# Optimization experiments

Hardware: AMD Instinct MI355X
Metric: run time of the kernel (lower is better)

## Reference

```python
import jax, jax.numpy as jnp
import numpy as np

B, N0, FEAT, NHID, GDIM = 32, 2048, 1036, 128, 32
DEG = 16
E = B * N0 * DEG
K1, K2, K3 = 410, 82, 17  # ceil(0.2*{2048,410,82}) per SAGPooling stage


def _segsum(v, idx, n):
    return jax.ops.segment_sum(v, idx, num_segments=n)


def sage_conv(x, src, dst, em, Wl, bl, Wr, n):
    # PyG SAGEConv: lin_l(mean_{j->i} x_j) + lin_r(x_i); lin applied before the
    # (linear) mean -> identical math, messages are NHID-dim not FEAT-dim.
    h = x @ Wl
    s = _segsum(h[src] * em[:, None], dst, n)
    cnt = _segsum(em, dst, n)
    return s / jnp.maximum(cnt, 1.0)[:, None] + bl + x @ Wr


def gcn_score(x, src, dst, em, W, b, n):
    # 1-channel GCNConv with self-loops and symmetric normalization.
    h = x @ W  # [n, 1]
    deg = 1.0 + _segsum(em, dst, n)  # +1 for self loop
    dis = jax.lax.rsqrt(deg)
    norm = dis[src] * dis[dst] * em
    agg = _segsum(h[src] * norm[:, None], dst, n) + h / deg[:, None]
    return (agg + b)[:, 0]


def sag_pool(x, src, dst, em, W, b, n_per, k):
    # Equal-size graphs -> static top-k per graph; dropped edges masked, not removed.
    nb = x.shape[0] // n_per
    score = gcn_score(x, src, dst, em, W, b, x.shape[0])
    _, idx = jax.lax.top_k(score.reshape(nb, n_per), k)
    perm = (idx + (jnp.arange(nb) * n_per)[:, None]).reshape(-1)
    xn = x[perm] * jnp.tanh(score[perm])[:, None]
    inv = jnp.full((x.shape[0],), -1, jnp.int32).at[perm].set(
        jnp.arange(nb * k, dtype=jnp.int32))
    ns, nd = inv[src], inv[dst]
    emn = em * ((ns >= 0) & (nd >= 0)).astype(em.dtype)
    return xn, jnp.maximum(ns, 0), jnp.maximum(nd, 0), emn


def readout(x, k):
    r = x.reshape(B, k, NHID)
    return jnp.concatenate([r.max(axis=1), r.mean(axis=1)], axis=1)  # [B, 2*NHID]


def graphnet(x, src, dst, W1l, b1l, W1r, Wp1, bp1, W2l, b2l, W2r, Wp2, bp2,
             W3l, b3l, W3r, Wp3, bp3, lin1_w, lin1_b, lin2_w, lin2_b, lin3_w, lin3_b):
    # NormalizeFeaturesV2: first 12 cols / column max
    mx = jnp.max(x[:, :12], axis=0)
    x = jnp.concatenate([x[:, :12] / mx, x[:, 12:]], axis=1)
    em = jnp.ones((E,), x.dtype)

    x = jax.nn.relu(sage_conv(x, src, dst, em, W1l, b1l, W1r, B * N0))
    x, s1, d1, e1 = sag_pool(x, src, dst, em, Wp1, bp1, N0, K1)
    x1 = readout(x, K1)

    x = jax.nn.relu(sage_conv(x, s1, d1, e1, W2l, b2l, W2r, B * K1))
    x, s2, d2, e2 = sag_pool(x, s1, d1, e1, Wp2, bp2, K1, K2)
    x2 = readout(x, K2)

    x = jax.nn.relu(sage_conv(x, s2, d2, e2, W3l, b3l, W3r, B * K2))
    x, s3, d3, e3 = sag_pool(x, s2, d2, e2, Wp3, bp3, K2, K3)
    x3 = readout(x, K3)

    h = x1 + x2 + x3
    h = jax.nn.relu(h @ lin1_w + lin1_b)  # dropout is identity at eval
    features = jax.nn.relu(h @ lin2_w + lin2_b)
    out = features @ lin3_w + lin3_b  # act=None
    return features, out


def setup_inputs():
    key = jax.random.key(0)
    ks = jax.random.split(key, 16)
    x = jax.random.normal(ks[0], (B * N0, FEAT), jnp.float32)
    e = jax.random.randint(ks[1], (2, B, N0 * DEG), 0, N0)
    ei = (e + (jnp.arange(B) * N0)[None, :, None]).reshape(2, -1).astype(jnp.int32)

    def lin(k, fi, fo):
        return (jax.random.normal(k, (fi, fo), jnp.float32) / np.sqrt(fi)).astype(jnp.float32)

    z = lambda *s: jnp.zeros(s, jnp.float32)
    return dict(
        x=x, src=ei[0], dst=ei[1],
        W1l=lin(ks[2], FEAT, NHID), b1l=z(NHID), W1r=lin(ks[3], FEAT, NHID),
        Wp1=lin(ks[4], NHID, 1), bp1=z(1),
        W2l=lin(ks[5], NHID, NHID), b2l=z(NHID), W2r=lin(ks[6], NHID, NHID),
        Wp2=lin(ks[7], NHID, 1), bp2=z(1),
        W3l=lin(ks[8], NHID, NHID), b3l=z(NHID), W3r=lin(ks[9], NHID, NHID),
        Wp3=lin(ks[10], NHID, 1), bp3=z(1),
        lin1_w=lin(ks[11], 2 * NHID, NHID), lin1_b=z(NHID),
        lin2_w=lin(ks[12], NHID, GDIM), lin2_b=z(GDIM),
        lin3_w=lin(ks[13], GDIM, 1), lin3_b=z(1),
    )


def reference(x, src, dst, W1l, b1l, W1r, Wp1, bp1, W2l, b2l, W2r, Wp2, bp2,
              W3l, b3l, W3r, Wp3, bp3, lin1_w, lin1_b, lin2_w, lin2_b, lin3_w, lin3_b):
    return graphnet(x, src, dst, W1l, b1l, W1r, Wp1, bp1, W2l, b2l, W2r, Wp2, bp2,
                    W3l, b3l, W3r, Wp3, bp3, lin1_w, lin1_b, lin2_w, lin2_b,
                    lin3_w, lin3_b)
```

## Files before the change

kernel.cpp:

```cpp
#include <hip/hip_runtime.h>

typedef unsigned int u32;
typedef unsigned short u16;

#define NB 32
#define N0V 2048
#define FEATV 1036
#define EDGESV (NB*N0V*16)
#define KK1 410
#define KK2 82
#define KK3 17
#define NN1 (NB*N0V)
#define NN2 (NB*KK1)
#define NN3 (NB*KK2)
#define NN4 (NB*KK3)
#define KSTEP1 33
#define KSTEP2 4
#define ESTR 32768

typedef __bf16 bf16x8 __attribute__((ext_vector_type(8)));
typedef float f32x4 __attribute__((ext_vector_type(4)));

__device__ inline u16 f2bf(float f){
  u32 u = __float_as_uint(f);
  u32 r = (u + 0x7FFFu + ((u >> 16) & 1u)) >> 16;
  return (u16)r;
}
__device__ inline float bf2f(u16 h){ return __uint_as_float(((u32)h) << 16); }
__device__ inline float dec_ord(u32 u){
  u32 bits = (u & 0x80000000u) ? (u ^ 0x80000000u) : ~u;
  return __uint_as_float(bits);
}
__device__ inline u16 bfbits(__bf16 b){ union{__bf16 f; u16 u;} c; c.f=b; return c.u; }
__device__ inline void cvt4c(float4 v, ushort4& h, ushort4& l){
  __bf16 h0=(__bf16)v.x, h1=(__bf16)v.y, h2=(__bf16)v.z, h3=(__bf16)v.w;
  float r0=v.x-(float)h0, r1=v.y-(float)h1, r2=v.z-(float)h2, r3=v.w-(float)h3;
  h.x=bfbits(h0); h.y=bfbits(h1); h.z=bfbits(h2); h.w=bfbits(h3);
  l.x=bfbits((__bf16)r0); l.y=bfbits((__bf16)r1);
  l.z=bfbits((__bf16)r2); l.w=bfbits((__bf16)r3);
}
__device__ inline void gload_lds16(const void* g, void* l){
  __builtin_amdgcn_global_load_lds(
      (const __attribute__((address_space(1))) unsigned int*)g,
      (__attribute__((address_space(3))) unsigned int*)l, 16, 0, 0);
}

__global__ void init_kernel(u32* mx){
  if (threadIdx.x < 12) mx[threadIdx.x] = 0;
}

__global__ void colmax_kernel(const float* __restrict__ x, u32* mx){
  __shared__ float sm[256];
  int t = threadIdx.x;
  int r = blockIdx.x*256 + t;
  const float4* p = (const float4*)(x + (size_t)r*FEATV);
  float4 v0 = p[0], v1 = p[1], v2 = p[2];
  float m[12] = {v0.x,v0.y,v0.z,v0.w, v1.x,v1.y,v1.z,v1.w, v2.x,v2.y,v2.z,v2.w};
  for (int j=0;j<12;j++){
    sm[t] = m[j]; __syncthreads();
    for (int off=128; off>0; off>>=1){ if (t<off) sm[t]=fmaxf(sm[t],sm[t+off]); __syncthreads(); }
    if (t==0){
      u32 b = __float_as_uint(sm[0]);
      u32 u = (b & 0x80000000u) ? ~b : (b | 0x80000000u);
      atomicMax(&mx[j], u);
    }
    __syncthreads();
  }
}

__global__ void wprep_all(const float* __restrict__ W1l, const float* __restrict__ W1r,
                          const float* __restrict__ W2l, const float* __restrict__ W2r,
                          const float* __restrict__ W3l, const float* __restrict__ W3r,
                          const u32* __restrict__ mxo,
                          u16* __restrict__ B1h, u16* __restrict__ B1l,
                          u16* __restrict__ B2h, u16* __restrict__ B2l,
                          u16* __restrict__ B3h, u16* __restrict__ B3l){
  int idx = blockIdx.x*256 + threadIdx.x;
  const float *Wl, *Wr; u16 *oh, *ol; int K, o, scale12;
  if (idx < KSTEP1*8192){ Wl=W1l; Wr=W1r; oh=B1h; ol=B1l; K=FEATV; o=idx; scale12=1; }
  else if (idx < (KSTEP1+KSTEP2)*8192){ Wl=W2l; Wr=W2r; oh=B2h; ol=B2l; K=128; o=idx-KSTEP1*8192; scale12=0; }
  else if (idx < (KSTEP1+2*KSTEP2)*8192){ Wl=W3l; Wr=W3r; oh=B3h; ol=B3l; K=128; o=idx-(KSTEP1+KSTEP2)*8192; scale12=0; }
  else return;
  int kt = o >> 13, r13 = o & 8191;
  int khg = r13 >> 11, n = (r13 >> 3) & 255, kk8 = r13 & 7;
  int k = (kt << 5) + khg*8 + kk8;
  float v = 0.f;
  if (k < K) v = (n < 128) ? Wl[(size_t)k*128 + n] : Wr[(size_t)k*128 + (n-128)];
  if (scale12 && k < 12) v /= dec_ord(mxo[k]);
  u16 h = f2bf(v);
  oh[o] = h;
  ol[o] = f2bf(v - bf2f(h));
}

__launch_bounds__(256, 3)
__global__ void gemm_csr_kernel(const float* __restrict__ A, int lda, int M,
                                int Kvalid, int Ksteps,
                                const u16* __restrict__ Bth, const u16* __restrict__ Btl,
                                float* __restrict__ C,
                                const int* __restrict__ sE, const int* __restrict__ dE,
                                const int* ecnt_in, int inGlobal, int nperIn, int nperOut,
                                const int* __restrict__ inv,
                                int* __restrict__ rps, int* __restrict__ rpd,
                                int* __restrict__ adjO, int* __restrict__ odstO,
                                int* __restrict__ ecnt_out){
  __shared__ __align__(16) u16 Ah[2][2048];
  __shared__ __align__(16) u16 Al[2][2048];
  __shared__ __align__(16) u16 Bhs[2][8192];
  int tid = threadIdx.x;

  if ((int)blockIdx.x < NB){
    int g = blockIdx.x;
    int* cnt  = (int*)&Bhs[0][0];
    int* part = (int*)&Ah[0][0];
    int ne = ecnt_in ? ecnt_in[g] : ESTR;
    size_t eb = (size_t)g*ESTR;
    for (int i = tid; i < nperOut; i += 256) cnt[i] = 0;
    __syncthreads();
    for (int e = tid; e < ne; e += 256){
      int s = sE[eb+e], d = dE[eb+e];
      int ld;
      bool ok;
      if (inv){
        int gs = inGlobal ? s : g*nperIn + s;
        int gd = inGlobal ? d : g*nperIn + d;
        int ls = inv[gs]; ld = inv[gd];
        ok = (ls >= 0) && (ld >= 0);
      } else { ld = d - g*nperIn; ok = true; }
      if (ok) atomicAdd(&cnt[ld], 1);
    }
    __syncthreads();
    int chunk = (nperOut + 255) >> 8;
    int c0 = tid*chunk, ssum = 0;
    for (int u = 0; u < chunk; ++u){ int i = c0+u; if (i < nperOut) ssum += cnt[i]; }
    part[tid] = ssum;
    __syncthreads();
    for (int off = 1; off < 256; off <<= 1){
      int v = (tid >= off) ? part[tid-off] : 0;
      __syncthreads();
      part[tid] += v;
      __syncthreads();
    }
    int total = part[255];
    int run = part[tid] - ssum;
    for (int u = 0; u < chunk; ++u){
      int i = c0+u;
      if (i < nperOut){
        int c = cnt[i];
        rps[g*nperOut + i] = (int)(g*ESTR + run);
        rpd[g*nperOut + i] = c;
        cnt[i] = run;
        run += c;
      }
    }
    __syncthreads();
    for (int e = tid; e < ne; e += 256){
      int s = sE[eb+e], d = dE[eb+e];
      int ls, ld;
      bool ok;
      if (inv){
        int gs = inGlobal ? s : g*nperIn + s;
        int gd = inGlobal ? d : g*nperIn + d;
        ls = inv[gs]; ld = inv[gd];
        ok = (ls >= 0) && (ld >= 0);
      } else { ls = s - g*nperIn; ld = d - g*nperIn; ok = true; }
      if (ok){
        int p = atomicAdd(&cnt[ld], 1);
        adjO[eb + p] = ls;
        if (odstO) odstO[eb + p] = ld;
      }
    }
    if (ecnt_out && tid == 0) ecnt_out[g] = total;
    return;
  }

  int row0 = ((int)blockIdx.x - NB) * 64;
  int w = tid >> 6, lane = tid & 63;
  int lr = lane & 15, kh = lane >> 4;

  int p0i = tid, p1i = tid + 256;
  int kg0 = p0i >> 7, rw0 = (p0i & 127) >> 1, hf0 = p0i & 1;
  int kg1 = p1i >> 7, rw1 = (p1i & 127) >> 1, hf1 = p1i & 1;
  int coff0 = kg0*8 + hf0*4, coff1 = kg1*8 + hf1*4;
  const float* pA0 = A + (size_t)(row0 + rw0)*lda + coff0;
  const float* pA1 = A + (size_t)(row0 + rw1)*lda + coff1;
  int wi0 = kg0*512 + rw0*8 + hf0*4;
  int wi1 = kg1*512 + rw1*8 + hf1*4;

  const u16* bpl = Btl + kh*2048 + (w*64 + lr)*8;

  f32x4 acc[4][4];
  #pragma unroll
  for (int i=0;i<4;i++)
    #pragma unroll
    for (int j=0;j<4;j++) acc[i][j] = (f32x4){0.f,0.f,0.f,0.f};

  float4 z4 = make_float4(0.f,0.f,0.f,0.f);
  bf16x8 blv[4];

#define LOADA(KT, V0, V1) { int k0_ = (KT)<<5; \
    V0 = (k0_ + coff0 < Kvalid) ? *(const float4*)(pA0 + k0_) : z4; \
    V1 = (k0_ + coff1 < Kvalid) ? *(const float4*)(pA1 + k0_) : z4; }

#define LOADBL(KT) { const u16* p_ = bpl + (size_t)(KT)*8192; \
    _Pragma("unroll") for (int ni_=0;ni_<4;ni_++) blv[ni_] = *(const bf16x8*)(p_ + ni_*128); }

#define ISSUEB(KT, BUF) { size_t tb_ = (size_t)(KT)*8192; \
    _Pragma("unroll") \
    for (int j_=0;j_<4;j_++){ int o_ = j_*2048 + w*512; \
      gload_lds16(Bth + tb_ + o_ + lane*8, &Bhs[BUF][o_]); } }

#define CVTWRITE(V0, V1, BUF) { ushort4 h_, l_; \
    cvt4c(V0, h_, l_); *(ushort4*)&Ah[BUF][wi0] = h_; *(ushort4*)&Al[BUF][wi0] = l_; \
    cvt4c(V1, h_, l_); *(ushort4*)&Ah[BUF][wi1] = h_; *(ushort4*)&Al[BUF][wi1] = l_; }

#define BODY(KT) { \
    LOADBL(KT);                                            \
    if ((KT)+1 < Ksteps) ISSUEB((KT)+1, ((KT)+1)&1);       \
    float4 n0 = z4, n1 = z4; \
    if ((KT)+2 < Ksteps) LOADA((KT)+2, n0, n1);            \
    int cur_ = (KT) & 1, nxt_ = cur_ ^ 1; \
    bf16x8 fah[4], fal[4], fbh[4]; \
    _Pragma("unroll") \
    for (int mi_=0;mi_<4;mi_++){ \
      int idx_ = kh*512 + (mi_*16 + lr)*8; \
      fah[mi_] = *(const bf16x8*)&Ah[cur_][idx_]; \
      fal[mi_] = *(const bf16x8*)&Al[cur_][idx_]; \
    } \
    _Pragma("unroll") \
    for (int ni_=0;ni_<4;ni_++){ \
      int idx_ = kh*2048 + (w*64 + ni_*16 + lr)*8; \
      fbh[ni_] = *(const bf16x8*)&Bhs[cur_][idx_]; \
    } \
    if ((KT)+1 < Ksteps) CVTWRITE(pp0, pp1, nxt_);         \
    asm volatile("s_waitcnt lgkmcnt(4)" ::: "memory");     \
    __builtin_amdgcn_sched_barrier(0); \
    __builtin_amdgcn_s_setprio(1); \
    _Pragma("unroll") \
    for (int mi_=0;mi_<4;mi_++) \
      _Pragma("unroll") \
      for (int ni_=0;ni_<4;ni_++){ \
        acc[mi_][ni_] = __builtin_amdgcn_mfma_f32_16x16x32_bf16(fah[mi_], fbh[ni_], acc[mi_][ni_], 0,0,0); \
        acc[mi_][ni_] = __builtin_amdgcn_mfma_f32_16x16x32_bf16(fal[mi_], fbh[ni_], acc[mi_][ni_], 0,0,0); \
      } \
    __builtin_amdgcn_s_setprio(0); \
    if ((KT)+2 < Ksteps)      { asm volatile("s_waitcnt vmcnt(6)" ::: "memory"); } \
    else if ((KT)+1 < Ksteps) { asm volatile("s_waitcnt vmcnt(4)" ::: "memory"); } \
    else                      { asm volatile("s_waitcnt vmcnt(0)" ::: "memory"); } \
    __builtin_amdgcn_sched_barrier(0); \
    __builtin_amdgcn_s_setprio(1); \
    _Pragma("unroll") \
    for (int mi_=0;mi_<4;mi_++) \
      _Pragma("unroll") \
      for (int ni_=0;ni_<4;ni_++) \
        acc[mi_][ni_] = __builtin_amdgcn_mfma_f32_16x16x32_bf16(fah[mi_], blv[ni_], acc[mi_][ni_], 0,0,0); \
    __builtin_amdgcn_s_setprio(0); \
    pp0 = n0; pp1 = n1; \
    asm volatile("s_waitcnt lgkmcnt(0)" ::: "memory"); \
    if ((KT)+2 < Ksteps)      { asm volatile("s_waitcnt vmcnt(2)" ::: "memory"); } \
    else                      { asm volatile("s_waitcnt vmcnt(0)" ::: "memory"); } \
    __builtin_amdgcn_s_barrier(); \
  }

  float4 a0, a1, pp0, pp1;
  LOADA(0, a0, a1);
  LOADA(1, pp0, pp1);
  ISSUEB(0, 0);
  CVTWRITE(a0, a1, 0);
  asm volatile("s_waitcnt lgkmcnt(0)" ::: "memory");
  asm volatile("s_waitcnt vmcnt(0)" ::: "memory");
  __builtin_amdgcn_s_barrier();

  for (int kt = 0; kt < Ksteps; ++kt) BODY(kt);
#undef LOADA
#undef LOADBL
#undef ISSUEB
#undef CVTWRITE
#undef BODY
  #pragma unroll
  for (int mi=0;mi<4;mi++)
    #pragma unroll
    for (int j=0;j<4;j++){
      int row = row0 + mi*16 + kh*4 + j;
      #pragma unroll
      for (int ni=0;ni<4;ni++){
        int col = w*64 + ni*16 + lr;
        C[(size_t)row*256 + col] = acc[mi][ni][j];
      }
    }
}

__global__ void convfin_w(const float* __restrict__ hcomb, const int* __restrict__ rps,
                          const int* __restrict__ rpd, const int* __restrict__ adj,
                          const float* __restrict__ bl, const float* __restrict__ Wp,
                          float* __restrict__ xout, float* __restrict__ hsc,
                          int nper, int bpg, int xcdMap){
  int b = blockIdx.x, t = threadIdx.x;
  int g, slot;
  if (xcdMap){ int xcd = b & 7, idx = b >> 3; g = xcd + 8*(idx >> 8); slot = idx & 255; }
  else { g = b / bpg; slot = b - g*bpg; }
  int wv = t >> 6, lane = t & 63;
  int sub = lane >> 5, l32 = lane & 31;
  int i = slot*8 + wv*2 + sub;
  if (i >= nper) return;
  int gbase = g*nper;
  int gi = gbase + i;
  int s = rps[gi], d = rpd[gi];
  float4 a = make_float4(0.f,0.f,0.f,0.f);
  #pragma unroll 4
  for (int e = s; e < s+d; ++e){
    float4 hj = *(const float4*)(hcomb + (size_t)(gbase + adj[e])*256 + l32*4);
    a.x += hj.x; a.y += hj.y; a.z += hj.z; a.w += hj.w;
  }
  float invc = 1.0f / fmaxf((float)d, 1.0f);
  float4 hr = *(const float4*)(hcomb + (size_t)gi*256 + 128 + l32*4);
  float4 bb = *(const float4*)(bl + l32*4);
  float4 o;
  o.x = fmaxf(a.x*invc + bb.x + hr.x, 0.f);
  o.y = fmaxf(a.y*invc + bb.y + hr.y, 0.f);
  o.z = fmaxf(a.z*invc + bb.z + hr.z, 0.f);
  o.w = fmaxf(a.w*invc + bb.w + hr.w, 0.f);
  *(float4*)(xout + (size_t)gi*128 + l32*4) = o;
  float4 wp = *(const float4*)(Wp + l32*4);
  float v = o.x*wp.x + o.y*wp.y + o.z*wp.z + o.w*wp.w;
  #pragma unroll
  for (int m = 16; m > 0; m >>= 1) v += __shfl_xor(v, m);
  if (l32 == 0) hsc[gi] = v;
}

__global__ void scoreagg_w(const float* __restrict__ hsc, const int* __restrict__ rps,
                           const int* __restrict__ rpd, const int* __restrict__ adj,
                           const float* __restrict__ bp, int nper,
                           u32* __restrict__ su){
  int g = blockIdx.y;
  int i = blockIdx.x*256 + threadIdx.x;
  if (i >= nper) return;
  int gbase = g*nper;
  int gi = gbase + i;
  float di = 1.0f + (float)rpd[gi];
  float a = hsc[gi] / di;
  float rdi = rsqrtf(di);
  int s = rps[gi], d = rpd[gi];
  #pragma unroll 4
  for (int e = s; e < s+d; ++e){
    int j = gbase + adj[e];
    a += hsc[j] * rsqrtf(1.0f + (float)rpd[j]) * rdi;
  }
  float sc = a + bp[0];
  u32 b = __float_as_uint(sc);
  su[gi] = (b & 0x80000000u) ? ~b : (b | 0x80000000u);
}

__launch_bounds__(512)
__global__ void topkpool(const u32* __restrict__ suG, const float* __restrict__ xin,
                         int nper, int k,
                         float* __restrict__ xp, float* __restrict__ r,
                         int* __restrict__ invG){
  __shared__ u32 su[2048];
  __shared__ int bins[256], sfx[256];
  __shared__ int slist[416];
  __shared__ int tlist[64];
  __shared__ float smx[512], ssm[512];
  __shared__ u32 spfx;
  __shared__ int srem, ssel, stie;
  int g = blockIdx.x, t = threadIdx.x;
  int gbase = g*nper;
  for (int i = t; i < nper; i += 512){
    su[i] = suG[gbase + i];
    invG[gbase + i] = -1;
  }
  if (t == 0){ spfx = 0; srem = k; ssel = 0; stie = 0; }
  __syncthreads();
  for (int pass = 0; pass < 4; ++pass){
    int shift = 24 - 8*pass;
    if (t < 256) bins[t] = 0;
    __syncthreads();
    u32 pfx = spfx; int rem = srem;
    for (int i = t; i < nper; i += 512){
      u32 u = su[i];
      if (pass == 0 || (u >> (shift+8)) == (pfx >> (shift+8)))
        atomicAdd(&bins[(u >> shift) & 255], 1);
    }
    __syncthreads();
    if (t < 256) sfx[t] = bins[t];
    __syncthreads();
    for (int off=1; off<256; off<<=1){
      int v = 0;
      if (t < 256 && t + off < 256) v = sfx[t+off];
      __syncthreads();
      if (t < 256) sfx[t] += v;
      __syncthreads();
    }
    if (t < 256){
      int above = (t == 255) ? 0 : sfx[t+1];
      if (sfx[t] >= rem && above < rem){
        spfx = pfx | ((u32)t << shift);
        srem = rem - above;
      }
    }
    __syncthreads();
  }
  u32 th = spfx;
  for (int i = t; i < nper; i += 512)
    if (su[i] > th){ int p = atomicAdd(&ssel, 1); slist[p] = i; }
  __syncthreads();
  for (int i = t; i < nper; i += 512)
    if (su[i] == th){ int q = atomicAdd(&stie, 1); if (q < 64) tlist[q] = i; }
  __syncthreads();
  if (t == 0){
    int p = ssel, need = k - p;
    if (need > 0){
      if (stie <= 64){
        for (int a = 1; a < stie; ++a){
          int v = tlist[a], b2 = a-1;
          while (b2 >= 0 && tlist[b2] > v){ tlist[b2+1] = tlist[b2]; b2--; }
          tlist[b2+1] = v;
        }
        for (int m = 0; m < need; ++m) slist[p+m] = tlist[m];
      } else {
        for (int i = 0; i < nper && p < k; ++i)
          if (su[i] == th) slist[p++] = i;
      }
    }
  }
  __syncthreads();
  int q = t >> 7, c = t & 127;
  float mxv = -3.4e38f, smv = 0.f;
  for (int j = q; j < k; j += 4){
    int li = slist[j];
    float ts = tanhf(dec_ord(su[li]));
    float vv = xin[((size_t)(gbase + li))*128 + c] * ts;
    xp[((size_t)(g*k + j))*128 + c] = vv;
    mxv = fmaxf(mxv, vv); smv += vv;
  }
  smx[t] = mxv; ssm[t] = smv;
  for (int j = t; j < k; j += 512) invG[gbase + slist[j]] = j;
  __syncthreads();
  if (t < 128){
    r[g*256 + t] = fmaxf(fmaxf(smx[t], smx[t+128]), fmaxf(smx[t+256], smx[t+384]));
    r[g*256 + 128 + t] = (ssm[t]+ssm[t+128]+ssm[t+256]+ssm[t+384]) / (float)k;
  }
}

__global__ void head_kernel(const float* __restrict__ r1, const float* __restrict__ r2,
                            const float* __restrict__ r3,
                            const float* __restrict__ w1, const float* __restrict__ b1,
                            const float* __restrict__ w2, const float* __restrict__ b2,
                            const float* __restrict__ w3, const float* __restrict__ b3,
                            float* __restrict__ out){
  __shared__ float hs[32][256];
  __shared__ float h1[32][128];
  __shared__ float ft[32][32];
  int t = threadIdx.x;
  for (int o = t; o < 32*256; o += 256) hs[o>>8][o&255] = r1[o]+r2[o]+r3[o];
  __syncthreads();
  for (int o = t; o < 32*128; o += 256){
    int i = o >> 7, j = o & 127;
    float a = b1[j];
    for (int c = 0; c < 256; ++c) a += hs[i][c]*w1[c*128 + j];
    h1[i][j] = fmaxf(a, 0.f);
  }
  __syncthreads();
  for (int o = t; o < 32*32; o += 256){
    int i = o >> 5, j = o & 31;
    float a = b2[j];
    for (int c = 0; c < 128; ++c) a += h1[i][c]*w2[c*32 + j];
    float v = fmaxf(a, 0.f);
    ft[i][j] = v;
    out[o] = v;
  }
  __syncthreads();
  if (t < 32){
    float a = b3[0];
    for (int c = 0; c < 32; ++c) a += ft[t][c]*w3[c];
    out[1024 + t] = a;
  }
}

extern "C" void kernel_launch(void* const* d_in, const int* in_sizes, int n_in,
                              void* d_out, int out_size, void* d_ws, size_t ws_size,
                              hipStream_t stream){
  (void)in_sizes; (void)n_in; (void)out_size; (void)ws_size;
  const float* x   = (const float*)d_in[0];
  const int* esrc  = (const int*)d_in[1];
  const int* edst  = (const int*)d_in[2];
  const float* W1l = (const float*)d_in[3];
  const float* b1l = (const float*)d_in[4];
  const float* W1r = (const float*)d_in[5];
  const float* Wp1 = (const float*)d_in[6];
  const float* bp1 = (const float*)d_in[7];
  const float* W2l = (const float*)d_in[8];
  const float* b2l = (const float*)d_in[9];
  const float* W2r = (const float*)d_in[10];
  const float* Wp2 = (const float*)d_in[11];
  const float* bp2 = (const float*)d_in[12];
  const float* W3l = (const float*)d_in[13];
  const float* b3l = (const float*)d_in[14];
  const float* W3r = (const float*)d_in[15];
  const float* Wp3 = (const float*)d_in[16];
  const float* bp3 = (const float*)d_in[17];
  const float* l1w = (const float*)d_in[18];
  const float* l1b = (const float*)d_in[19];
  const float* l2w = (const float*)d_in[20];
  const float* l2b = (const float*)d_in[21];
  const float* l3w = (const float*)d_in[22];
  const float* l3b = (const float*)d_in[23];
  float* out = (float*)d_out;

  char* ws = (char*)d_ws;
  size_t off = 0;
  auto alloc = [&](size_t bytes)->char*{
    char* p = ws + off; off = (off + bytes + 255) & ~(size_t)255; return p;
  };

  u32* mx     = (u32*)alloc(64);
  int* ecntA  = (int*)alloc(NB*4);
  int* rps   = (int*)alloc((size_t)NN1*4);
  int* rpd   = (int*)alloc((size_t)NN1*4);
  int* adj1  = (int*)alloc((size_t)EDGESV*4);
  int* adjA  = (int*)alloc((size_t)EDGESV*4);
  int* odstA = (int*)alloc((size_t)EDGESV*4);
  int* adjB  = (int*)alloc((size_t)EDGESV*4);
  u16* B1h   = (u16*)alloc((size_t)KSTEP1*8192*2);
  u16* B1l   = (u16*)alloc((size_t)KSTEP1*8192*2);
  u16* B2h   = (u16*)alloc((size_t)KSTEP2*8192*2);
  u16* B2l   = (u16*)alloc((size_t)KSTEP2*8192*2);
  u16* B3h   = (u16*)alloc((size_t)KSTEP2*8192*2);
  u16* B3l   = (u16*)alloc((size_t)KSTEP2*8192*2);
  float* hcomb = (float*)alloc((size_t)NN1*256*4);
  float* x1    = (float*)alloc((size_t)NN1*128*4);
  float* x2    = (float*)alloc((size_t)NN2*128*4);
  float* x3    = (float*)alloc((size_t)NN3*128*4);
  float* xp1   = (float*)alloc((size_t)NN2*128*4);
  float* xp2   = (float*)alloc((size_t)NN3*128*4);
  float* xp3   = (float*)alloc((size_t)NN4*128*4);
  float* hsc   = (float*)alloc((size_t)NN1*4);
  u32* suG     = (u32*)alloc((size_t)NN1*4);
  int* invG    = (int*)alloc((size_t)NN1*4);
  float* r1    = (float*)alloc((size_t)32*256*4);
  float* r2    = (float*)alloc((size_t)32*256*4);
  float* r3    = (float*)alloc((size_t)32*256*4);

  init_kernel<<<1, 64, 0, stream>>>(mx);
  colmax_kernel<<<256, 256, 0, stream>>>(x, mx);
  wprep_all<<<((KSTEP1+2*KSTEP2)*8192+255)/256, 256, 0, stream>>>(
      W1l, W1r, W2l, W2r, W3l, W3r, mx, B1h, B1l, B2h, B2l, B3h, B3l);

  gemm_csr_kernel<<<NB + NN1/64, 256, 0, stream>>>(
      x, FEATV, NN1, FEATV, KSTEP1, B1h, B1l, hcomb,
      esrc, edst, nullptr, 1, N0V, N0V, nullptr,
      rps, rpd, adj1, nullptr, nullptr);
  convfin_w<<<NN1/8, 256, 0, stream>>>(hcomb, rps, rpd, adj1, b1l, Wp1, x1, hsc, N0V, 256, 1);
  scoreagg_w<<<dim3(N0V/256, NB), 256, 0, stream>>>(hsc, rps, rpd, adj1, bp1, N0V, suG);
  topkpool<<<NB, 512, 0, stream>>>(suG, x1, N0V, KK1, xp1, r1, invG);

  gemm_csr_kernel<<<NB + NN2/64, 256, 0, stream>>>(
      xp1, 128, NN2, 128, KSTEP2, B2h, B2l, hcomb,
      esrc, edst, nullptr, 1, N0V, KK1, invG,
      rps, rpd, adjA, odstA, ecntA);
  convfin_w<<<NB*52, 256, 0, stream>>>(hcomb, rps, rpd, adjA, b2l, Wp2, x2, hsc, KK1, 52, 0);
  scoreagg_w<<<dim3((KK1+255)/256, NB), 256, 0, stream>>>(hsc, rps, rpd, adjA, bp2, KK1, suG);
  topkpool<<<NB, 512, 0, stream>>>(suG, x2, KK1, KK2, xp2, r2, invG);

  gemm_csr_kernel<<<NB + NN3/64, 256, 0, stream>>>(
      xp2, 128, NN3, 128, KSTEP2, B3h, B3l, hcomb,
      adjA, odstA, ecntA, 0, KK1, KK2, invG,
      rps, rpd, adjB, nullptr, nullptr);
  convfin_w<<<NB*11, 256, 0, stream>>>(hcomb, rps, rpd, adjB, b3l, Wp3, x3, hsc, KK2, 11, 0);
  scoreagg_w<<<dim3(1, NB), 256, 0, stream>>>(hsc, rps, rpd, adjB, bp3, KK2, suG);
  topkpool<<<NB, 512, 0, stream>>>(suG, x3, KK2, KK3, xp3, r3, invG);

  head_kernel<<<1, 256, 0, stream>>>(r1, r2, r3, l1w, l1b, l2w, l2b, l3w, l3b, out);
}
```

Baseline: 574.2 us.

## Stage B low half in LDS, split GEMM output, fuse score aggregation into top-k

The GEMM main loop now stages both the high and low bf16 halves of the weights into LDS through async global-to-LDS loads. Previously the low half was read straight from global into registers, and the loop used split waits between two MFMA phases. Launch bounds drop from 3 to 2 blocks per SM to fit the doubled B buffers. The output is written to separate hl/hr buffers with 128-wide rows, which halves the row stride that convfin gathers through. The score aggregation kernel is merged into the top-k pooling kernel, removing a launch and a global round trip, though the per-graph work now runs on only 32 blocks.

```diff
diff --git a/kernel.cpp b/kernel.cpp
--- a/kernel.cpp
+++ b/kernel.cpp
@@ -92,11 +92,11 @@
   ol[o] = f2bf(v - bf2f(h));
 }
 
-__launch_bounds__(256, 3)
+__launch_bounds__(256, 2)
 __global__ void gemm_csr_kernel(const float* __restrict__ A, int lda, int M,
                                 int Kvalid, int Ksteps,
                                 const u16* __restrict__ Bth, const u16* __restrict__ Btl,
-                                float* __restrict__ C,
+                                float* __restrict__ hl, float* __restrict__ hr,
                                 const int* __restrict__ sE, const int* __restrict__ dE,
                                 const int* ecnt_in, int inGlobal, int nperIn, int nperOut,
                                 const int* __restrict__ inv,
@@ -105,12 +105,13 @@
                                 int* __restrict__ ecnt_out){
   __shared__ __align__(16) u16 Ah[2][2048];
   __shared__ __align__(16) u16 Al[2][2048];
-  __shared__ __align__(16) u16 Bhs[2][8192];
+  __shared__ __align__(16) u16 Bh[2][8192];
+  __shared__ __align__(16) u16 Bl[2][8192];
   int tid = threadIdx.x;
 
   if ((int)blockIdx.x < NB){
     int g = blockIdx.x;
-    int* cnt  = (int*)&Bhs[0][0];
+    int* cnt  = (int*)&Bh[0][0];
     int* part = (int*)&Ah[0][0];
     int ne = ecnt_in ? ecnt_in[g] : ESTR;
     size_t eb = (size_t)g*ESTR;
@@ -118,8 +119,7 @@
     __syncthreads();
     for (int e = tid; e < ne; e += 256){
       int s = sE[eb+e], d = dE[eb+e];
-      int ld;
-      bool ok;
+      int ld; bool ok;
       if (inv){
         int gs = inGlobal ? s : g*nperIn + s;
         int gd = inGlobal ? d : g*nperIn + d;
@@ -155,8 +155,7 @@
     __syncthreads();
     for (int e = tid; e < ne; e += 256){
       int s = sE[eb+e], d = dE[eb+e];
-      int ls, ld;
-      bool ok;
+      int ls, ld; bool ok;
       if (inv){
         int gs = inGlobal ? s : g*nperIn + s;
         int gd = inGlobal ? d : g*nperIn + d;
@@ -186,8 +185,6 @@
   int wi0 = kg0*512 + rw0*8 + hf0*4;
   int wi1 = kg1*512 + rw1*8 + hf1*4;
 
-  const u16* bpl = Btl + kh*2048 + (w*64 + lr)*8;
-
   f32x4 acc[4][4];
   #pragma unroll
   for (int i=0;i<4;i++)
@@ -195,87 +192,72 @@
     for (int j=0;j<4;j++) acc[i][j] = (f32x4){0.f,0.f,0.f,0.f};
 
   float4 z4 = make_float4(0.f,0.f,0.f,0.f);
-  bf16x8 blv[4];
 
 #define LOADA(KT, V0, V1) { int k0_ = (KT)<<5; \
     V0 = (k0_ + coff0 < Kvalid) ? *(const float4*)(pA0 + k0_) : z4; \
     V1 = (k0_ + coff1 < Kvalid) ? *(const float4*)(pA1 + k0_) : z4; }
 
-#define LOADBL(KT) { const u16* p_ = bpl + (size_t)(KT)*8192; \
-    _Pragma("unroll") for (int ni_=0;ni_<4;ni_++) blv[ni_] = *(const bf16x8*)(p_ + ni_*128); }
-
 #define ISSUEB(KT, BUF) { size_t tb_ = (size_t)(KT)*8192; \
     _Pragma("unroll") \
     for (int j_=0;j_<4;j_++){ int o_ = j_*2048 + w*512; \
-      gload_lds16(Bth + tb_ + o_ + lane*8, &Bhs[BUF][o_]); } }
+      gload_lds16(Bth + tb_ + o_ + lane*8, &Bh[BUF][o_]); \
+      gload_lds16(Btl + tb_ + o_ + lane*8, &Bl[BUF][o_]); } }
 
 #define CVTWRITE(V0, V1, BUF) { ushort4 h_, l_; \
     cvt4c(V0, h_, l_); *(ushort4*)&Ah[BUF][wi0] = h_; *(ushort4*)&Al[BUF][wi0] = l_; \
     cvt4c(V1, h_, l_); *(ushort4*)&Ah[BUF][wi1] = h_; *(ushort4*)&Al[BUF][wi1] = l_; }
 
-#define BODY(KT) { \
-    LOADBL(KT);                                            \
-    if ((KT)+1 < Ksteps) ISSUEB((KT)+1, ((KT)+1)&1);       \
-    float4 n0 = z4, n1 = z4; \
-    if ((KT)+2 < Ksteps) LOADA((KT)+2, n0, n1);            \
-    int cur_ = (KT) & 1, nxt_ = cur_ ^ 1; \
-    bf16x8 fah[4], fal[4], fbh[4]; \
-    _Pragma("unroll") \
-    for (int mi_=0;mi_<4;mi_++){ \
-      int idx_ = kh*512 + (mi_*16 + lr)*8; \
-      fah[mi_] = *(const bf16x8*)&Ah[cur_][idx_]; \
-      fal[mi_] = *(const bf16x8*)&Al[cur_][idx_]; \
-    } \
-    _Pragma("unroll") \
-    for (int ni_=0;ni_<4;ni_++){ \
-      int idx_ = kh*2048 + (w*64 + ni_*16 + lr)*8; \
-      fbh[ni_] = *(const bf16x8*)&Bhs[cur_][idx_]; \
-    } \
-    if ((KT)+1 < Ksteps) CVTWRITE(pp0, pp1, nxt_);         \
-    asm volatile("s_waitcnt lgkmcnt(4)" ::: "memory");     \
-    __builtin_amdgcn_sched_barrier(0); \
-    __builtin_amdgcn_s_setprio(1); \
-    _Pragma("unroll") \
-    for (int mi_=0;mi_<4;mi_++) \
-      _Pragma("unroll") \
-      for (int ni_=0;ni_<4;ni_++){ \
-        acc[mi_][ni_] = __builtin_amdgcn_mfma_f32_16x16x32_bf16(fah[mi_], fbh[ni_], acc[mi_][ni_], 0,0,0); \
-        acc[mi_][ni_] = __builtin_amdgcn_mfma_f32_16x16x32_bf16(fal[mi_], fbh[ni_], acc[mi_][ni_], 0,0,0); \
-      } \
-    __builtin_amdgcn_s_setprio(0); \
-    if ((KT)+2 < Ksteps)      { asm volatile("s_waitcnt vmcnt(6)" ::: "memory"); } \
-    else if ((KT)+1 < Ksteps) { asm volatile("s_waitcnt vmcnt(4)" ::: "memory"); } \
-    else                      { asm volatile("s_waitcnt vmcnt(0)" ::: "memory"); } \
-    __builtin_amdgcn_sched_barrier(0); \
-    __builtin_amdgcn_s_setprio(1); \
-    _Pragma("unroll") \
-    for (int mi_=0;mi_<4;mi_++) \
-      _Pragma("unroll") \
-      for (int ni_=0;ni_<4;ni_++) \
-        acc[mi_][ni_] = __builtin_amdgcn_mfma_f32_16x16x32_bf16(fah[mi_], blv[ni_], acc[mi_][ni_], 0,0,0); \
-    __builtin_amdgcn_s_setprio(0); \
-    pp0 = n0; pp1 = n1; \
-    asm volatile("s_waitcnt lgkmcnt(0)" ::: "memory"); \
-    if ((KT)+2 < Ksteps)      { asm volatile("s_waitcnt vmcnt(2)" ::: "memory"); } \
-    else                      { asm volatile("s_waitcnt vmcnt(0)" ::: "memory"); } \
-    __builtin_amdgcn_s_barrier(); \
-  }
-
   float4 a0, a1, pp0, pp1;
   LOADA(0, a0, a1);
+  ISSUEB(0, 0);
   LOADA(1, pp0, pp1);
-  ISSUEB(0, 0);
   CVTWRITE(a0, a1, 0);
   asm volatile("s_waitcnt lgkmcnt(0)" ::: "memory");
-  asm volatile("s_waitcnt vmcnt(0)" ::: "memory");
+  asm volatile("s_waitcnt vmcnt(2)" ::: "memory");
   __builtin_amdgcn_s_barrier();
 
-  for (int kt = 0; kt < Ksteps; ++kt) BODY(kt);
+  for (int kt = 0; kt < Ksteps; ++kt){
+    int cur = kt & 1, nxt = cur ^ 1;
+    if (kt+1 < Ksteps) ISSUEB(kt+1, nxt);
+    float4 n0 = z4, n1 = z4;
+    if (kt+2 < Ksteps) LOADA(kt+2, n0, n1);
+    if (kt+2 < Ksteps)      asm volatile("s_waitcnt vmcnt(12)" ::: "memory");
+    else if (kt+1 < Ksteps) asm volatile("s_waitcnt vmcnt(10)" ::: "memory");
+    else                    asm volatile("s_waitcnt vmcnt(0)"  ::: "memory");
+
+    bf16x8 fah[4], fal[4], fbh[4], fbl[4];
+    #pragma unroll
+    for (int mi=0;mi<4;mi++){
+      int idx = kh*512 + (mi*16 + lr)*8;
+      fah[mi] = *(const bf16x8*)&Ah[cur][idx];
+      fal[mi] = *(const bf16x8*)&Al[cur][idx];
+    }
+    #pragma unroll
+    for (int ni=0;ni<4;ni++){
+      int idx = kh*2048 + (w*64 + ni*16 + lr)*8;
+      fbh[ni] = *(const bf16x8*)&Bh[cur][idx];
+      fbl[ni] = *(const bf16x8*)&Bl[cur][idx];
+    }
+    if (kt+1 < Ksteps) CVTWRITE(pp0, pp1, nxt);
+    asm volatile("s_waitcnt lgkmcnt(0)" ::: "memory");
+    __builtin_amdgcn_sched_barrier(0);
+    __builtin_amdgcn_s_setprio(1);
+    #pragma unroll
+    for (int mi=0;mi<4;mi++)
+      #pragma unroll
+      for (int ni=0;ni<4;ni++){
+        acc[mi][ni] = __builtin_amdgcn_mfma_f32_16x16x32_bf16(fah[mi], fbh[ni], acc[mi][ni], 0,0,0);
+        acc[mi][ni] = __builtin_amdgcn_mfma_f32_16x16x32_bf16(fah[mi], fbl[ni], acc[mi][ni], 0,0,0);
+        acc[mi][ni] = __builtin_amdgcn_mfma_f32_16x16x32_bf16(fal[mi], fbh[ni], acc[mi][ni], 0,0,0);
+      }
+    __builtin_amdgcn_s_setprio(0);
+    pp0 = n0; pp1 = n1;
+    __builtin_amdgcn_s_barrier();
+  }
 #undef LOADA
-#undef LOADBL
 #undef ISSUEB
 #undef CVTWRITE
-#undef BODY
+  float* dst = (w < 2) ? hl : hr;
   #pragma unroll
   for (int mi=0;mi<4;mi++)
     #pragma unroll
@@ -283,13 +265,14 @@
       int row = row0 + mi*16 + kh*4 + j;
       #pragma unroll
       for (int ni=0;ni<4;ni++){
-        int col = w*64 + ni*16 + lr;
-        C[(size_t)row*256 + col] = acc[mi][ni][j];
+        int ch = (w*64 + ni*16 + lr) & 127;
+        dst[(size_t)row*128 + ch] = acc[mi][ni][j];
       }
     }
 }
 
-__global__ void convfin_w(const float* __restrict__ hcomb, const int* __restrict__ rps,
+__global__ void convfin_w(const float* __restrict__ hl, const float* __restrict__ hr,
+                          const int* __restrict__ rps,
                           const int* __restrict__ rpd, const int* __restrict__ adj,
                           const float* __restrict__ bl, const float* __restrict__ Wp,
                           float* __restrict__ xout, float* __restrict__ hsc,
@@ -308,17 +291,17 @@
   float4 a = make_float4(0.f,0.f,0.f,0.f);
   #pragma unroll 4
   for (int e = s; e < s+d; ++e){
-    float4 hj = *(const float4*)(hcomb + (size_t)(gbase + adj[e])*256 + l32*4);
+    float4 hj = *(const float4*)(hl + (size_t)(gbase + adj[e])*128 + l32*4);
     a.x += hj.x; a.y += hj.y; a.z += hj.z; a.w += hj.w;
   }
   float invc = 1.0f / fmaxf((float)d, 1.0f);
-  float4 hr = *(const float4*)(hcomb + (size_t)gi*256 + 128 + l32*4);
+  float4 hrv = *(const float4*)(hr + (size_t)gi*128 + l32*4);
   float4 bb = *(const float4*)(bl + l32*4);
   float4 o;
-  o.x = fmaxf(a.x*invc + bb.x + hr.x, 0.f);
-  o.y = fmaxf(a.y*invc + bb.y + hr.y, 0.f);
-  o.z = fmaxf(a.z*invc + bb.z + hr.z, 0.f);
-  o.w = fmaxf(a.w*invc + bb.w + hr.w, 0.f);
+  o.x = fmaxf(a.x*invc + bb.x + hrv.x, 0.f);
+  o.y = fmaxf(a.y*invc + bb.y + hrv.y, 0.f);
+  o.z = fmaxf(a.z*invc + bb.z + hrv.z, 0.f);
+  o.w = fmaxf(a.w*invc + bb.w + hrv.w, 0.f);
   *(float4*)(xout + (size_t)gi*128 + l32*4) = o;
   float4 wp = *(const float4*)(Wp + l32*4);
   float v = o.x*wp.x + o.y*wp.y + o.z*wp.z + o.w*wp.w;
@@ -327,32 +310,11 @@
   if (l32 == 0) hsc[gi] = v;
 }
 
-__global__ void scoreagg_w(const float* __restrict__ hsc, const int* __restrict__ rps,
-                           const int* __restrict__ rpd, const int* __restrict__ adj,
-                           const float* __restrict__ bp, int nper,
-                           u32* __restrict__ su){
-  int g = blockIdx.y;
-  int i = blockIdx.x*256 + threadIdx.x;
-  if (i >= nper) return;
-  int gbase = g*nper;
-  int gi = gbase + i;
-  float di = 1.0f + (float)rpd[gi];
-  float a = hsc[gi] / di;
-  float rdi = rsqrtf(di);
-  int s = rps[gi], d = rpd[gi];
-  #pragma unroll 4
-  for (int e = s; e < s+d; ++e){
-    int j = gbase + adj[e];
-    a += hsc[j] * rsqrtf(1.0f + (float)rpd[j]) * rdi;
-  }
-  float sc = a + bp[0];
-  u32 b = __float_as_uint(sc);
-  su[gi] = (b & 0x80000000u) ? ~b : (b | 0x80000000u);
-}
-
 __launch_bounds__(512)
-__global__ void topkpool(const u32* __restrict__ suG, const float* __restrict__ xin,
-                         int nper, int k,
+__global__ void pooltail(const float* __restrict__ hsc, const int* __restrict__ rps,
+                         const int* __restrict__ rpd, const int* __restrict__ adj,
+                         const float* __restrict__ bp,
+                         const float* __restrict__ xin, int nper, int k,
                          float* __restrict__ xp, float* __restrict__ r,
                          int* __restrict__ invG){
   __shared__ u32 su[2048];
@@ -364,9 +326,21 @@
   __shared__ int srem, ssel, stie;
   int g = blockIdx.x, t = threadIdx.x;
   int gbase = g*nper;
+  float bpv = bp[0];
   for (int i = t; i < nper; i += 512){
-    su[i] = suG[gbase + i];
-    invG[gbase + i] = -1;
+    int gi = gbase + i;
+    invG[gi] = -1;
+    float di = 1.0f + (float)rpd[gi];
+    float a = hsc[gi] / di;
+    float rdi = rsqrtf(di);
+    int s = rps[gi], d = rpd[gi];
+    for (int e = s; e < s+d; ++e){
+      int j = gbase + adj[e];
+      a += hsc[j] * rsqrtf(1.0f + (float)rpd[j]) * rdi;
+    }
+    float sc = a + bpv;
+    u32 b = __float_as_uint(sc);
+    su[i] = (b & 0x80000000u) ? ~b : (b | 0x80000000u);
   }
   if (t == 0){ spfx = 0; srem = k; ssel = 0; stie = 0; }
   __syncthreads();
@@ -526,7 +500,8 @@
   u16* B2l   = (u16*)alloc((size_t)KSTEP2*8192*2);
   u16* B3h   = (u16*)alloc((size_t)KSTEP2*8192*2);
   u16* B3l   = (u16*)alloc((size_t)KSTEP2*8192*2);
-  float* hcomb = (float*)alloc((size_t)NN1*256*4);
+  float* hlb = (float*)alloc((size_t)NN1*128*4);
+  float* hrb = (float*)alloc((size_t)NN1*128*4);
   float* x1    = (float*)alloc((size_t)NN1*128*4);
   float* x2    = (float*)alloc((size_t)NN2*128*4);
   float* x3    = (float*)alloc((size_t)NN3*128*4);
@@ -534,7 +509,6 @@
   float* xp2   = (float*)alloc((size_t)NN3*128*4);
   float* xp3   = (float*)alloc((size_t)NN4*128*4);
   float* hsc   = (float*)alloc((size_t)NN1*4);
-  u32* suG     = (u32*)alloc((size_t)NN1*4);
   int* invG    = (int*)alloc((size_t)NN1*4);
   float* r1    = (float*)alloc((size_t)32*256*4);
   float* r2    = (float*)alloc((size_t)32*256*4);
@@ -546,28 +520,25 @@
       W1l, W1r, W2l, W2r, W3l, W3r, mx, B1h, B1l, B2h, B2l, B3h, B3l);
 
   gemm_csr_kernel<<<NB + NN1/64, 256, 0, stream>>>(
-      x, FEATV, NN1, FEATV, KSTEP1, B1h, B1l, hcomb,
+      x, FEATV, NN1, FEATV, KSTEP1, B1h, B1l, hlb, hrb,
       esrc, edst, nullptr, 1, N0V, N0V, nullptr,
       rps, rpd, adj1, nullptr, nullptr);
-  convfin_w<<<NN1/8, 256, 0, stream>>>(hcomb, rps, rpd, adj1, b1l, Wp1, x1, hsc, N0V, 256, 1);
-  scoreagg_w<<<dim3(N0V/256, NB), 256, 0, stream>>>(hsc, rps, rpd, adj1, bp1, N0V, suG);
-  topkpool<<<NB, 512, 0, stream>>>(suG, x1, N0V, KK1, xp1, r1, invG);
+  convfin_w<<<NN1/8, 256, 0, stream>>>(hlb, hrb, rps, rpd, adj1, b1l, Wp1, x1, hsc, N0V, 256, 1);
+  pooltail<<<NB, 512, 0, stream>>>(hsc, rps, rpd, adj1, bp1, x1, N0V, KK1, xp1, r1, invG);
 
   gemm_csr_kernel<<<NB + NN2/64, 256, 0, stream>>>(
-      xp1, 128, NN2, 128, KSTEP2, B2h, B2l, hcomb,
+      xp1, 128, NN2, 128, KSTEP2, B2h, B2l, hlb, hrb,
       esrc, edst, nullptr, 1, N0V, KK1, invG,
       rps, rpd, adjA, odstA, ecntA);
-  convfin_w<<<NB*52, 256, 0, stream>>>(hcomb, rps, rpd, adjA, b2l, Wp2, x2, hsc, KK1, 52, 0);
-  scoreagg_w<<<dim3((KK1+255)/256, NB), 256, 0, stream>>>(hsc, rps, rpd, adjA, bp2, KK1, suG);
-  topkpool<<<NB, 512, 0, stream>>>(suG, x2, KK1, KK2, xp2, r2, invG);
+  convfin_w<<<NB*52, 256, 0, stream>>>(hlb, hrb, rps, rpd, adjA, b2l, Wp2, x2, hsc, KK1, 52, 0);
+  pooltail<<<NB, 512, 0, stream>>>(hsc, rps, rpd, adjA, bp2, x2, KK1, KK2, xp2, r2, invG);
 
   gemm_csr_kernel<<<NB + NN3/64, 256, 0, stream>>>(
-      xp2, 128, NN3, 128, KSTEP2, B3h, B3l, hcomb,
+      xp2, 128, NN3, 128, KSTEP2, B3h, B3l, hlb, hrb,
       adjA, odstA, ecntA, 0, KK1, KK2, invG,
       rps, rpd, adjB, nullptr, nullptr);
-  convfin_w<<<NB*11, 256, 0, stream>>>(hcomb, rps, rpd, adjB, b3l, Wp3, x3, hsc, KK2, 11, 0);
-  scoreagg_w<<<dim3(1, NB), 256, 0, stream>>>(hsc, rps, rpd, adjB, bp3, KK2, suG);
-  topkpool<<<NB, 512, 0, stream>>>(suG, x3, KK2, KK3, xp3, r3, invG);
+  convfin_w<<<NB*11, 256, 0, stream>>>(hlb, hrb, rps, rpd, adjB, b3l, Wp3, x3, hsc, KK2, 11, 0);
+  pooltail<<<NB, 512, 0, stream>>>(hsc, rps, rpd, adjB, bp3, x3, KK2, KK3, xp3, r3, invG);
 
   head_kernel<<<1, 256, 0, stream>>>(r1, r2, r3, l1w, l1b, l2w, l2b, l3w, l3b, out);
 }
```

Result: faster. 551.1 us (-4.0%).
